# Optimization experiments

Hardware: AMD Instinct MI355X
Metric: run time of the kernel (lower is better)

The kernel has to match this reference:

```python
import jax, jax.numpy as jnp
import numpy as np

H, W = 512, 512
NUM_CLASSES = 21
THETA_ALPHA, THETA_BETA, THETA_GAMMA = 80.0, 13.0, 3.0
BILATERAL_COMPAT, SPATIAL_COMPAT = 10.0, 3.0
COMPATIBILITY = -1.0
NUM_ITERATIONS = 5


def _find_rows(rows, queries):
    """Index of each query row in `rows` (lexicographically sorted unique), -1 if absent."""
    M = rows.shape[0]
    u, inv = np.unique(np.concatenate([rows, queries], axis=0), axis=0, return_inverse=True)
    table = np.full(u.shape[0], -1, np.int64)
    table[inv[:M]] = np.arange(M)
    return table[inv[M:]].astype(np.int32)


def _perm_init(feats):
    """Permutohedral lattice init (Adams et al.).
    Returns os [N,d+1] (1-based lattice indices, 0 = pad row), ws [N,d+1] barycentric
    weights, nbrs [d+1,M,2] blur neighbor indices (1-based, 0 = missing)."""
    N, d = feats.shape
    inv_std = np.sqrt(2.0 / 3.0) * (d + 1)
    scale = inv_std / np.sqrt((np.arange(1, d + 1) * np.arange(2, d + 2)).astype(np.float64))
    cf = feats.astype(np.float64) * scale[None]
    # Elevate onto the hyperplane sum(x)=0 in d+1 dims
    E = np.zeros((N, d + 1), np.float64)
    sm = np.zeros(N, np.float64)
    for i in range(d, 0, -1):
        E[:, i] = sm - i * cf[:, i - 1]
        sm = sm + cf[:, i - 1]
    E[:, 0] = sm
    down = 1.0 / (d + 1)
    v = E * down
    up_p = np.ceil(v) * (d + 1)
    dn_p = np.floor(v) * (d + 1)
    rem0 = np.where(up_p - E < E - dn_p, up_p, dn_p)  # nearest remainder-0 point
    sum_ = np.round(rem0.sum(1) * down).astype(np.int64)
    diff = E - rem0
    order = np.argsort(-diff, axis=1, kind='stable')
    rank = np.empty((N, d + 1), np.int64)
    np.put_along_axis(rank, order, np.broadcast_to(np.arange(d + 1, dtype=np.int64), (N, d + 1)).copy(), axis=1)
    rank = rank + sum_[:, None]
    ls = rank < 0
    rank = rank + ls * (d + 1); rem0 = rem0 + ls * (d + 1)
    gt = rank > d
    rank = rank - gt * (d + 1); rem0 = rem0 - gt * (d + 1)
    # Barycentric weights
    bary = np.zeros((N, d + 2), np.float64)
    vv = (E - rem0) * down
    rows_idx = np.arange(N)[:, None]
    np.add.at(bary, (rows_idx, d - rank), vv)
    np.add.at(bary, (rows_idx, d + 1 - rank), -vv)
    bary[:, 0] += 1.0 + bary[:, d + 1]
    ws = bary[:, :d + 1].astype(np.float32)
    # Keys of the d+1 enclosing simplex vertices (first d coords only)
    rem0i = np.round(rem0[:, :d]).astype(np.int32)
    ranks = rank[:, :d]
    keys = np.empty((N, d + 1, d), np.int32)
    for k in range(d + 1):
        keys[:, k, :] = rem0i + np.where(ranks < d + 1 - k, k, k - (d + 1)).astype(np.int32)
    uniq, inv = np.unique(keys.reshape(-1, d), axis=0, return_inverse=True)
    M = uniq.shape[0]
    os_ = (inv.reshape(N, d + 1) + 1).astype(np.int32)
    # Blur neighbors along each lattice direction j
    nbrs = np.zeros((d + 1, M, 2), np.int32)
    for j in range(d + 1):
        n1 = uniq - 1; n2 = uniq + 1
        if j < d:
            n1 = n1.copy(); n2 = n2.copy()
            n1[:, j] += d + 1; n2[:, j] -= d + 1
        nbrs[j, :, 0] = _find_rows(uniq, n1) + 1
        nbrs[j, :, 1] = _find_rows(uniq, n2) + 1
    return os_, ws, nbrs


def setup_inputs() -> dict:
    key = jax.random.key(0)
    k1, k2 = jax.random.split(key)
    unary = jax.random.normal(k1, (H, W, NUM_CLASSES), jnp.float32)
    image = jax.random.uniform(k2, (H, W, 3), jnp.float32) * 255.0  # 0..255 like RGB
    ys, xs = np.meshgrid(np.arange(H, dtype=np.float32), np.arange(W, dtype=np.float32), indexing='ij')
    img = np.asarray(image)
    bifeats = np.concatenate([(xs / THETA_ALPHA)[..., None], (ys / THETA_ALPHA)[..., None], img / THETA_BETA], axis=-1).reshape(-1, 5).astype(np.float32)
    spfeats = np.concatenate([(xs / THETA_GAMMA)[..., None], (ys / THETA_GAMMA)[..., None]], axis=-1).reshape(-1, 2).astype(np.float32)
    os_bi, ws_bi, nbr_bi = _perm_init(bifeats)
    os_sp, ws_sp, nbr_sp = _perm_init(spfeats)
    return {
        'unary': unary,
        'ws_bi': jnp.asarray(ws_bi), 'ws_sp': jnp.asarray(ws_sp),
        'os_bi': jnp.asarray(os_bi), 'os_sp': jnp.asarray(os_sp),
        'nbr_bi': jnp.asarray(nbr_bi), 'nbr_sp': jnp.asarray(nbr_sp),
    }


def lattice_compute(inp, os_, ws, nbrs):
    """Permutohedral splat -> blur -> slice. inp [N,C]; os_ [N,d+1] 1-based;
    ws [N,d+1]; nbrs [d+1,M,2] 1-based with 0 = missing (maps to zero pad row)."""
    N, C = inp.shape
    d = os_.shape[1] - 1
    M = nbrs.shape[1]
    splat = (ws[..., None] * inp[:, None, :]).reshape(-1, C)  # [N*(d+1), C]
    val = jnp.zeros((M + 1, C), inp.dtype).at[os_.reshape(-1)].add(splat)

    def blur(val, nbr_j):
        mixed = val[1:] + 0.5 * (val[nbr_j[:, 0]] + val[nbr_j[:, 1]])
        return val.at[1:].set(mixed), None

    val, _ = jax.lax.scan(blur, val, nbrs)
    alpha = 1.0 / (1.0 + 2.0 ** (-d))
    return alpha * jnp.einsum('nj,njc->nc', ws, val[os_])


def reference(unary, ws_bi, ws_sp, os_bi, os_sp, nbr_bi, nbr_sp):
    N = H * W
    u = unary.reshape(N, NUM_CLASSES)
    ones = jnp.ones((N, 1), jnp.float32)
    bi_norm = 1.0 / (lattice_compute(ones, os_bi, ws_bi, nbr_bi) ** 0.5 + 1e-20)
    sp_norm = 1.0 / (lattice_compute(ones, os_sp, ws_sp, nbr_sp) ** 0.5 + 1e-20)
    Q = jax.nn.softmax(-u, axis=-1)
    for _ in range(NUM_ITERATIONS):
        bi = lattice_compute(Q * bi_norm, os_bi, ws_bi, nbr_bi) * bi_norm
        sp = lattice_compute(Q * sp_norm, os_sp, ws_sp, nbr_sp) * sp_norm
        pairwise = COMPATIBILITY * (BILATERAL_COMPAT * bi + SPATIAL_COMPAT * sp)
        Q = jax.nn.softmax(-u - pairwise, axis=-1)
    return Q.reshape(H, W, NUM_CLASSES)
```

## Files before the change

kernel.cpp:

```cpp
#include <hip/hip_runtime.h>
#include <hip/hip_fp16.h>

#define NPIX (512 * 512)
#define LOG2N 18
#define NC 21
#define CP 11
#define SCAN_CHUNK 2048
#define SCAN_T 256

static inline int cdiv_l(long a, int b) { return (int)((a + b - 1) / b); }

__global__ void histrank2_k(const int* __restrict__ osA, int* __restrict__ cntA,
                            int* __restrict__ rnkA, int NA, int KA,
                            const int* __restrict__ osB, int* __restrict__ cntB,
                            int* __restrict__ rnkB, int NB, int KB) {
    int t = blockIdx.x * blockDim.x + threadIdx.x;
    if (t < NA) {
        int j = t >> LOG2N, n = t & (NPIX - 1);
        rnkA[t] = atomicAdd(&cntA[osA[(size_t)n * KA + j]], 1);
    } else {
        int tb = t - NA;
        if (tb < NB) {
            int j = tb >> LOG2N, n = tb & (NPIX - 1);
            rnkB[tb] = atomicAdd(&cntB[osB[(size_t)n * KB + j]], 1);
        }
    }
}

__global__ void scan1d_k(const int* __restrict__ cntA, int* __restrict__ bsumA, int LA, int nbA,
                         const int* __restrict__ cntB, int* __restrict__ bsumB, int LB) {
    __shared__ int s[SCAN_T];
    int blk = blockIdx.x;
    const int* cnt; int* bsum; int L; int b;
    if (blk < nbA) { cnt = cntA; bsum = bsumA; L = LA; b = blk; }
    else           { cnt = cntB; bsum = bsumB; L = LB; b = blk - nbA; }
    int base = b * SCAN_CHUNK;
    int tsum = 0;
    for (int j = threadIdx.x; j < SCAN_CHUNK; j += SCAN_T) {
        int i = base + j;
        tsum += (i < L) ? cnt[i] : 0;
    }
    s[threadIdx.x] = tsum; __syncthreads();
    for (int o = SCAN_T / 2; o > 0; o >>= 1) {
        if (threadIdx.x < o) s[threadIdx.x] += s[threadIdx.x + o];
        __syncthreads();
    }
    if (threadIdx.x == 0) bsum[b] = s[0];
}

__global__ void scan2d_k(int* __restrict__ bsumA, int nbA, int* __restrict__ offA, int LA,
                         int* __restrict__ bsumB, int nbB, int* __restrict__ offB, int LB) {
    __shared__ int s[SCAN_T];
    int* bsum; int nb; int* off; int L;
    if (blockIdx.x == 0) { bsum = bsumA; nb = nbA; off = offA; L = LA; }
    else                 { bsum = bsumB; nb = nbB; off = offB; L = LB; }
    int tid = threadIdx.x;
    int per = (nb + SCAN_T - 1) / SCAN_T;
    int tsum = 0;
    for (int j = 0; j < per; j++) { int i = tid * per + j; if (i < nb) tsum += bsum[i]; }
    s[tid] = tsum; __syncthreads();
    for (int o = 1; o < SCAN_T; o <<= 1) {
        int v = (tid >= o) ? s[tid - o] : 0;
        __syncthreads();
        s[tid] += v;
        __syncthreads();
    }
    int excl = s[tid] - tsum;
    int total = s[SCAN_T - 1];
    int run = excl;
    for (int j = 0; j < per; j++) {
        int i = tid * per + j;
        if (i < nb) { int v = bsum[i]; bsum[i] = run; run += v; }
    }
    if (tid == 0) off[L] = total;
}

__global__ void scan3d_k(const int* __restrict__ cntA, const int* __restrict__ bsumA,
                         int* __restrict__ offA, int LA, int nbA,
                         const int* __restrict__ cntB, const int* __restrict__ bsumB,
                         int* __restrict__ offB, int LB) {
    __shared__ int s[SCAN_T];
    const int PER = SCAN_CHUNK / SCAN_T;
    int blk = blockIdx.x;
    const int* cnt; const int* bsum; int* off; int L; int b;
    if (blk < nbA) { cnt = cntA; bsum = bsumA; off = offA; L = LA; b = blk; }
    else           { cnt = cntB; bsum = bsumB; off = offB; L = LB; b = blk - nbA; }
    int tid = threadIdx.x;
    int base = b * SCAN_CHUNK + tid * PER;
    int c[PER];
    int tsum = 0;
#pragma unroll
    for (int j = 0; j < PER; j++) { int i = base + j; c[j] = (i < L) ? cnt[i] : 0; tsum += c[j]; }
    s[tid] = tsum; __syncthreads();
    for (int o = 1; o < SCAN_T; o <<= 1) {
        int v = (tid >= o) ? s[tid - o] : 0;
        __syncthreads();
        s[tid] += v;
        __syncthreads();
    }
    int run = bsum[b] + s[tid] - tsum;
#pragma unroll
    for (int j = 0; j < PER; j++) {
        int i = base + j;
        if (i < L) off[i] = run;
        run += c[j];
    }
}

__global__ void scatter2_k(const int* __restrict__ osA, const float* __restrict__ wsA,
                           const int* __restrict__ offA, const int* __restrict__ rnkA,
                           int2* __restrict__ pA, int NA, int KA,
                           const int* __restrict__ osB, const float* __restrict__ wsB,
                           const int* __restrict__ offB, const int* __restrict__ rnkB,
                           int2* __restrict__ pB, int NB, int KB) {
    int t = blockIdx.x * blockDim.x + threadIdx.x;
    if (t < NA) {
        int j = t >> LOG2N, n = t & (NPIX - 1);
        size_t e = (size_t)n * KA + j;
        int m = osA[e];
        int p = offA[m] + rnkA[t];
        pA[p] = make_int2(n, __float_as_int(wsA[e]));
    } else {
        int tb = t - NA;
        if (tb < NB) {
            int j = tb >> LOG2N, n = tb & (NPIX - 1);
            size_t e = (size_t)n * KB + j;
            int m = osB[e];
            int p = offB[m] + rnkB[tb];
            pB[p] = make_int2(n, __float_as_int(wsB[e]));
        }
    }
}

__global__ void wn2_k(int2* __restrict__ pA, const float* __restrict__ nrmA, int NA,
                      int2* __restrict__ pB, const float* __restrict__ nrmB, int NB) {
    int t = blockIdx.x * blockDim.x + threadIdx.x;
    if (t < NA) {
        int2 e = pA[t];
        e.y = __float_as_int(__int_as_float(e.y) * nrmA[e.x]);
        pA[t] = e;
    } else {
        t -= NA;
        if (t < NB) {
            int2 e = pB[t];
            e.y = __float_as_int(__int_as_float(e.y) * nrmB[e.x]);
            pB[t] = e;
        }
    }
}

__global__ void splat1d_k(const int2* __restrict__ pE_bi, const int* __restrict__ off_bi,
                          float* __restrict__ val_bi, int Mbi,
                          const int2* __restrict__ pE_sp, const int* __restrict__ off_sp,
                          float* __restrict__ val_sp, int Msp) {
    int t = blockIdx.x * blockDim.x + threadIdx.x;
    const int2* pE; const int* off; float* val; int m;
    if (t <= Mbi) { pE = pE_bi; off = off_bi; val = val_bi; m = t; }
    else {
        m = t - (Mbi + 1);
        if (m > Msp) return;
        pE = pE_sp; off = off_sp; val = val_sp;
    }
    float s = 0.f;
    if (m > 0) {
        int e0 = off[m], e1 = off[m + 1];
        for (int e = e0; e < e1; e++) s += __int_as_float(pE[e].y);
    }
    val[m] = s;
}

__global__ void blur1d_k(const float* __restrict__ biIn, float* __restrict__ biOut,
                         const int* __restrict__ nbr_bi, int Mbi,
                         const float* __restrict__ spIn, float* __restrict__ spOut,
                         const int* __restrict__ nbr_sp, int Msp) {
    int t = blockIdx.x * blockDim.x + threadIdx.x;
    if (t <= Mbi) {
        if (t == 0) { biOut[0] = 0.f; return; }
        int2 nn = ((const int2*)nbr_bi)[t - 1];
        biOut[t] = biIn[t] + 0.5f * (biIn[nn.x] + biIn[nn.y]);
    } else if (spIn) {
        int m = t - (Mbi + 1);
        if (m > Msp) return;
        if (m == 0) { spOut[0] = 0.f; return; }
        int2 nn = ((const int2*)nbr_sp)[m - 1];
        spOut[m] = spIn[m] + 0.5f * (spIn[nn.x] + spIn[nn.y]);
    }
}

__global__ void prep_k(const float* __restrict__ unary,
                       const int* __restrict__ os_bi, const float* __restrict__ ws_bi,
                       const float* __restrict__ nv_bi, float* __restrict__ nrm_bi, float abi,
                       const int* __restrict__ os_sp, const float* __restrict__ ws_sp,
                       const float* __restrict__ nv_sp, float* __restrict__ nrm_sp, float asp,
                       __half2* __restrict__ Qh, __half2* __restrict__ uh, int N) {
    int t = blockIdx.x * blockDim.x + threadIdx.x;
    if (t < N) {
        float s = 0.f;
        for (int j = 0; j < 6; j++)
            s += ws_bi[(size_t)t * 6 + j] * nv_bi[os_bi[(size_t)t * 6 + j]];
        nrm_bi[t] = 1.f / (sqrtf(abi * s) + 1e-20f);
    } else if (t < 2 * N) {
        int n = t - N;
        float s = 0.f;
        for (int j = 0; j < 3; j++)
            s += ws_sp[(size_t)n * 3 + j] * nv_sp[os_sp[(size_t)n * 3 + j]];
        nrm_sp[n] = 1.f / (sqrtf(asp * s) + 1e-20f);
    } else if (t < 3 * N) {
        int n = t - 2 * N;
        const float* up = unary + (size_t)n * NC;
        float uv[2 * CP], v[2 * CP];
        float mx = -1e30f;
#pragma unroll
        for (int c = 0; c < NC; c++) { uv[c] = up[c]; v[c] = -uv[c]; mx = fmaxf(mx, v[c]); }
        float s = 0.f;
#pragma unroll
        for (int c = 0; c < NC; c++) { v[c] = __expf(v[c] - mx); s += v[c]; }
        float inv = 1.f / s;
#pragma unroll
        for (int c = 0; c < NC; c++) v[c] *= inv;
        v[NC] = 0.f; uv[NC] = 0.f;
        __half2* hp = Qh + (size_t)n * CP;
        __half2* uhp = uh + (size_t)n * CP;
#pragma unroll
        for (int i = 0; i < CP; i++) {
            hp[i]  = __floats2half2_rn(v[2 * i], v[2 * i + 1]);
            uhp[i] = __floats2half2_rn(uv[2 * i], uv[2 * i + 1]);
        }
    }
}

__device__ __forceinline__ void splat_row(const __half2* __restrict__ Qh,
                                          const int2* __restrict__ pE, const int* __restrict__ off,
                                          __half2* __restrict__ val, int m) {
    float acc[2 * CP];
#pragma unroll
    for (int i = 0; i < 2 * CP; i++) acc[i] = 0.f;
    if (m > 0) {
        int e0 = off[m], e1 = off[m + 1];
        for (int e = e0; e < e1; e++) {
            int2 ent = pE[e];
            float w = __int_as_float(ent.y);
            const __half2* qp = Qh + (size_t)ent.x * CP;
#pragma unroll
            for (int i = 0; i < CP; i++) {
                float2 q = __half22float2(qp[i]);
                acc[2 * i]     += w * q.x;
                acc[2 * i + 1] += w * q.y;
            }
        }
    }
    __half2* vp = val + (size_t)m * CP;
#pragma unroll
    for (int i = 0; i < CP; i++)
        vp[i] = __floats2half2_rn(acc[2 * i], acc[2 * i + 1]);
}

__global__ void splatH2_k(const __half2* __restrict__ Qh,
                          const int2* __restrict__ pE_bi, const int* __restrict__ off_bi,
                          __half2* __restrict__ val_bi, int Mbi,
                          const int2* __restrict__ pE_sp, const int* __restrict__ off_sp,
                          __half2* __restrict__ val_sp, int Msp) {
    int t = blockIdx.x * blockDim.x + threadIdx.x;
    if (t <= Mbi) {
        splat_row(Qh, pE_bi, off_bi, val_bi, t);
    } else {
        int m = t - (Mbi + 1);
        if (m > Msp) return;
        splat_row(Qh, pE_sp, off_sp, val_sp, m);
    }
}

__device__ __forceinline__ void blur2_row(const __half2* __restrict__ vin, __half2* __restrict__ op,
                                          const int* __restrict__ nbrA, const int* __restrict__ nbrB,
                                          int m) {
    if (m == 0) {
        __half2 z = __floats2half2_rn(0.f, 0.f);
#pragma unroll
        for (int i = 0; i < CP; i++) op[i] = z;
        return;
    }
    float acc[2 * CP];
#pragma unroll
    for (int i = 0; i < 2 * CP; i++) acc[i] = 0.f;
    int2 nbB = ((const int2*)nbrB)[m - 1];
    {
        int2 na = ((const int2*)nbrA)[m - 1];
        const __half2* p0 = vin + (size_t)m * CP;
        const __half2* p1 = vin + (size_t)na.x * CP;
        const __half2* p2 = vin + (size_t)na.y * CP;
#pragma unroll
        for (int i = 0; i < CP; i++) {
            float2 a = __half22float2(p0[i]);
            float2 b = __half22float2(p1[i]);
            float2 c = __half22float2(p2[i]);
            acc[2 * i]     += a.x + 0.5f * (b.x + c.x);
            acc[2 * i + 1] += a.y + 0.5f * (b.y + c.y);
        }
    }
    if (nbB.x > 0) {
        int2 na = ((const int2*)nbrA)[nbB.x - 1];
        const __half2* p0 = vin + (size_t)nbB.x * CP;
        const __half2* p1 = vin + (size_t)na.x * CP;
        const __half2* p2 = vin + (size_t)na.y * CP;
#pragma unroll
        for (int i = 0; i < CP; i++) {
            float2 a = __half22float2(p0[i]);
            float2 b = __half22float2(p1[i]);
            float2 c = __half22float2(p2[i]);
            acc[2 * i]     += 0.5f * (a.x + 0.5f * (b.x + c.x));
            acc[2 * i + 1] += 0.5f * (a.y + 0.5f * (b.y + c.y));
        }
    }
    if (nbB.y > 0) {
        int2 na = ((const int2*)nbrA)[nbB.y - 1];
        const __half2* p0 = vin + (size_t)nbB.y * CP;
        const __half2* p1 = vin + (size_t)na.x * CP;
        const __half2* p2 = vin + (size_t)na.y * CP;
#pragma unroll
        for (int i = 0; i < CP; i++) {
            float2 a = __half22float2(p0[i]);
            float2 b = __half22float2(p1[i]);
            float2 c = __half22float2(p2[i]);
            acc[2 * i]     += 0.5f * (a.x + 0.5f * (b.x + c.x));
            acc[2 * i + 1] += 0.5f * (a.y + 0.5f * (b.y + c.y));
        }
    }
#pragma unroll
    for (int i = 0; i < CP; i++)
        op[i] = __floats2half2_rn(acc[2 * i], acc[2 * i + 1]);
}

__device__ __forceinline__ void blur1_row(const __half2* __restrict__ vin, __half2* __restrict__ op,
                                          const int* __restrict__ nbr, int m) {
    if (m == 0) {
        __half2 z = __floats2half2_rn(0.f, 0.f);
#pragma unroll
        for (int i = 0; i < CP; i++) op[i] = z;
        return;
    }
    int2 nn = ((const int2*)nbr)[m - 1];
    const __half2* p0 = vin + (size_t)m * CP;
    const __half2* p1 = vin + (size_t)nn.x * CP;
    const __half2* p2 = vin + (size_t)nn.y * CP;
#pragma unroll
    for (int i = 0; i < CP; i++) {
        float2 a = __half22float2(p0[i]);
        float2 b = __half22float2(p1[i]);
        float2 c = __half22float2(p2[i]);
        op[i] = __floats2half2_rn(a.x + 0.5f * (b.x + c.x), a.y + 0.5f * (b.y + c.y));
    }
}

__global__ void blurP1_k(const __half2* __restrict__ biIn, __half2* __restrict__ biOut,
                         const int* __restrict__ nA_bi, const int* __restrict__ nB_bi, int Mbi,
                         const __half2* __restrict__ spIn, __half2* __restrict__ spOut,
                         const int* __restrict__ nA_sp, const int* __restrict__ nB_sp, int Msp) {
    int t = blockIdx.x * blockDim.x + threadIdx.x;
    if (t <= Mbi) {
        blur2_row(biIn, biOut + (size_t)t * CP, nA_bi, nB_bi, t);
    } else {
        int m = t - (Mbi + 1);
        if (m > Msp) return;
        blur2_row(spIn, spOut + (size_t)m * CP, nA_sp, nB_sp, m);
    }
}

__global__ void blurP2_k(const __half2* __restrict__ biIn, __half2* __restrict__ biOut,
                         const int* __restrict__ nA_bi, const int* __restrict__ nB_bi, int Mbi,
                         const __half2* __restrict__ spIn, __half2* __restrict__ spOut,
                         const int* __restrict__ nA_sp, int Msp) {
    int t = blockIdx.x * blockDim.x + threadIdx.x;
    if (t <= Mbi) {
        blur2_row(biIn, biOut + (size_t)t * CP, nA_bi, nB_bi, t);
    } else {
        int m = t - (Mbi + 1);
        if (m > Msp) return;
        blur1_row(spIn, spOut + (size_t)m * CP, nA_sp, m);
    }
}

__global__ void blurP3_k(const __half2* __restrict__ biIn, __half2* __restrict__ biOut,
                         const int* __restrict__ nA_bi, const int* __restrict__ nB_bi, int Mbi) {
    int t = blockIdx.x * blockDim.x + threadIdx.x;
    if (t > Mbi) return;
    blur2_row(biIn, biOut + (size_t)t * CP, nA_bi, nB_bi, t);
}

__global__ void slice_update_k(const __half2* __restrict__ uh,
                               const int* __restrict__ os_bi, const float* __restrict__ ws_bi,
                               const __half2* __restrict__ vbi, const float* __restrict__ nrm_bi,
                               const int* __restrict__ os_sp, const float* __restrict__ ws_sp,
                               const __half2* __restrict__ vsp, const float* __restrict__ nrm_sp,
                               float* __restrict__ Q, __half2* __restrict__ Qh,
                               int N, float abi, float asp, int final_it) {
    int n = blockIdx.x * blockDim.x + threadIdx.x;
    if (n >= N) return;
    float acc[2 * CP];
#pragma unroll
    for (int i = 0; i < 2 * CP; i++) acc[i] = 0.f;
    for (int j = 0; j < 6; j++) {
        float w = ws_bi[(size_t)n * 6 + j];
        const __half2* vp = vbi + (size_t)os_bi[(size_t)n * 6 + j] * CP;
#pragma unroll
        for (int i = 0; i < CP; i++) {
            float2 f = __half22float2(vp[i]);
            acc[2 * i]     += w * f.x;
            acc[2 * i + 1] += w * f.y;
        }
    }
    float sb = 10.f * abi * nrm_bi[n];
#pragma unroll
    for (int i = 0; i < 2 * CP; i++) acc[i] *= sb;
    float ss = 3.f * asp * nrm_sp[n];
    for (int j = 0; j < 3; j++) {
        float w = ss * ws_sp[(size_t)n * 3 + j];
        const __half2* vp = vsp + (size_t)os_sp[(size_t)n * 3 + j] * CP;
#pragma unroll
        for (int i = 0; i < CP; i++) {
            float2 f = __half22float2(vp[i]);
            acc[2 * i]     += w * f.x;
            acc[2 * i + 1] += w * f.y;
        }
    }
    const __half2* uhp = uh + (size_t)n * CP;
#pragma unroll
    for (int i = 0; i < CP; i++) {
        float2 uu = __half22float2(uhp[i]);
        acc[2 * i]     -= uu.x;
        acc[2 * i + 1] -= uu.y;
    }
    float mx = -1e30f;
#pragma unroll
    for (int c = 0; c < NC; c++) mx = fmaxf(mx, acc[c]);
    float s = 0.f;
#pragma unroll
    for (int c = 0; c < NC; c++) { acc[c] = __expf(acc[c] - mx); s += acc[c]; }
    float inv = 1.f / s;
#pragma unroll
    for (int c = 0; c < NC; c++) acc[c] *= inv;
    acc[NC] = 0.f;
    if (final_it) {
        float* qp = Q + (size_t)n * NC;
#pragma unroll
        for (int c = 0; c < NC; c++) qp[c] = acc[c];
    } else {
        __half2* hp = Qh + (size_t)n * CP;
#pragma unroll
        for (int i = 0; i < CP; i++) hp[i] = __floats2half2_rn(acc[2 * i], acc[2 * i + 1]);
    }
}

extern "C" void kernel_launch(void* const* d_in, const int* in_sizes, int n_in,
                              void* d_out, int out_size, void* d_ws, size_t ws_size,
                              hipStream_t stream) {
    const float* unary  = (const float*)d_in[0];
    const float* ws_bi  = (const float*)d_in[1];
    const float* ws_sp  = (const float*)d_in[2];
    const int*   os_bi  = (const int*)d_in[3];
    const int*   os_sp  = (const int*)d_in[4];
    const int*   nbr_bi = (const int*)d_in[5];
    const int*   nbr_sp = (const int*)d_in[6];
    float* Q = (float*)d_out;

    const int N = NPIX, Kbi = 6, Ksp = 3;
    const int Mbi = in_sizes[5] / (Kbi * 2);
    const int Msp = in_sizes[6] / (Ksp * 2);
    const int NKbi = N * Kbi, NKsp = N * Ksp;
    const float alpha_bi = 32.f / 33.f;
    const float alpha_sp = 0.8f;

    char* basec = (char*)d_ws;
    size_t off4 = 0;
    auto allocf = [&](size_t nf) { float* p = (float*)basec + off4; off4 += (nf + 3) & ~(size_t)3; return p; };
    auto alloci = [&](size_t ni) { int* p = (int*)basec + off4; off4 += (ni + 3) & ~(size_t)3; return p; };
    auto alloch2 = [&](size_t nh2) { __half2* p = (__half2*)((float*)basec + off4); off4 += (nh2 + 3) & ~(size_t)3; return p; };
    auto alloci2 = [&](size_t ni2) { int2* p = (int2*)((float*)basec + off4); off4 += 2 * ni2; return p; };

    float*   nrm_bi = allocf(N);
    float*   nrm_sp = allocf(N);
    __half2* Qh     = alloch2((size_t)N * CP);
    __half2* uh     = alloch2((size_t)N * CP);
    int2*    pE_bi  = alloci2(NKbi);
    int*     off_bi = alloci(Mbi + 2);
    int2*    pE_sp  = alloci2(NKsp);
    int*     off_sp = alloci(Msp + 2);
    int*     cnt_bi = alloci((size_t)(Mbi + 1) + (Msp + 1));
    int*     cnt_sp = cnt_bi + (Mbi + 1);
    int*     rnk_bi = alloci(NKbi);
    int*     rnk_sp = alloci(NKsp);
    int*     bsumA  = alloci(4096);
    int*     bsumB  = alloci(4096);
    __half2* vbiA   = alloch2((size_t)(Mbi + 1) * CP);
    __half2* vbiB   = alloch2((size_t)(Mbi + 1) * CP);
    __half2* vspA   = alloch2((size_t)(Msp + 1) * CP);
    __half2* vspB   = alloch2((size_t)(Msp + 1) * CP);
    float* nv_biA = (float*)vbiA;
    float* nv_biB = (float*)vbiB;
    float* nv_spA = (float*)vspA;
    float* nv_spB = (float*)vspB;

    const int B = 256;
    const int nb_bi = cdiv_l(Mbi + 1, SCAN_CHUNK);
    const int nb_sp = cdiv_l(Msp + 1, SCAN_CHUNK);
    const size_t cnt_span = ((size_t)(Mbi + 1) + (Msp + 1)) * sizeof(int);
    const int rows2 = (Mbi + 1) + (Msp + 1);

    hipMemsetAsync(cnt_bi, 0, cnt_span, stream);
    histrank2_k<<<cdiv_l((long)NKbi + NKsp, B), B, 0, stream>>>(
        os_bi, cnt_bi, rnk_bi, NKbi, Kbi, os_sp, cnt_sp, rnk_sp, NKsp, Ksp);
    scan1d_k<<<nb_bi + nb_sp, SCAN_T, 0, stream>>>(cnt_bi, bsumA, Mbi + 1, nb_bi,
                                                   cnt_sp, bsumB, Msp + 1);
    scan2d_k<<<2, SCAN_T, 0, stream>>>(bsumA, nb_bi, off_bi, Mbi + 1,
                                       bsumB, nb_sp, off_sp, Msp + 1);
    scan3d_k<<<nb_bi + nb_sp, SCAN_T, 0, stream>>>(cnt_bi, bsumA, off_bi, Mbi + 1, nb_bi,
                                                   cnt_sp, bsumB, off_sp, Msp + 1);
    scatter2_k<<<cdiv_l((long)NKbi + NKsp, B), B, 0, stream>>>(
        os_bi, ws_bi, off_bi, rnk_bi, pE_bi, NKbi, Kbi,
        os_sp, ws_sp, off_sp, rnk_sp, pE_sp, NKsp, Ksp);

    splat1d_k<<<cdiv_l(rows2, B), B, 0, stream>>>(pE_bi, off_bi, nv_biA, Mbi,
                                                  pE_sp, off_sp, nv_spA, Msp);
    {
        float* sb = nv_biA; float* db = nv_biB;
        float* sp = nv_spA; float* dp = nv_spB;
        for (int j = 0; j < 3; j++) {
            blur1d_k<<<cdiv_l(rows2, B), B, 0, stream>>>(
                sb, db, nbr_bi + (size_t)j * Mbi * 2, Mbi,
                sp, dp, nbr_sp + (size_t)j * Msp * 2, Msp);
            float* t = sb; sb = db; db = t;
            t = sp; sp = dp; dp = t;
        }
        for (int j = 3; j < 6; j++) {
            blur1d_k<<<cdiv_l(Mbi + 1, B), B, 0, stream>>>(
                sb, db, nbr_bi + (size_t)j * Mbi * 2, Mbi,
                nullptr, nullptr, nullptr, 0);
            float* t = sb; sb = db; db = t;
        }
        prep_k<<<cdiv_l(3L * N, B), B, 0, stream>>>(
            unary, os_bi, ws_bi, sb, nrm_bi, alpha_bi,
            os_sp, ws_sp, sp, nrm_sp, alpha_sp, Qh, uh, N);
    }

    wn2_k<<<cdiv_l((long)NKbi + NKsp, B), B, 0, stream>>>(pE_bi, nrm_bi, NKbi, pE_sp, nrm_sp, NKsp);

    for (int it = 0; it < 5; it++) {
        splatH2_k<<<cdiv_l(rows2, B), B, 0, stream>>>(
            Qh, pE_bi, off_bi, vbiA, Mbi,
            pE_sp, off_sp, vspA, Msp);
        blurP1_k<<<cdiv_l(rows2, B), B, 0, stream>>>(
            vbiA, vbiB, nbr_bi + (size_t)0 * Mbi * 2, nbr_bi + (size_t)1 * Mbi * 2, Mbi,
            vspA, vspB, nbr_sp + (size_t)0 * Msp * 2, nbr_sp + (size_t)1 * Msp * 2, Msp);
        blurP2_k<<<cdiv_l(rows2, B), B, 0, stream>>>(
            vbiB, vbiA, nbr_bi + (size_t)2 * Mbi * 2, nbr_bi + (size_t)3 * Mbi * 2, Mbi,
            vspB, vspA, nbr_sp + (size_t)2 * Msp * 2, Msp);
        blurP3_k<<<cdiv_l(Mbi + 1, B), B, 0, stream>>>(
            vbiA, vbiB, nbr_bi + (size_t)4 * Mbi * 2, nbr_bi + (size_t)5 * Mbi * 2, Mbi);
        slice_update_k<<<cdiv_l(N, B), B, 0, stream>>>(
            uh, os_bi, ws_bi, vbiB, nrm_bi, os_sp, ws_sp, vspA, nrm_sp,
            Q, Qh, N, alpha_bi, alpha_sp, it == 4 ? 1 : 0);
    }
}
```

Baseline: 1.083 ms.

## Parallelize splat and blur kernels over lattice rows and channel pairs

The splat and blur kernels now launch one thread per (lattice row, half2 channel pair) instead of one thread per row, giving about eleven times more threads. Neighbor gathers become coalesced across adjacent threads reading consecutive half2 values of the same row, and per-thread register pressure drops. In exchange, each thread reloads the row's offsets, neighbor indices and splat entries, so index traffic is duplicated across the eleven channel threads, and an integer divide by CP is added per thread.

```diff
diff --git a/kernel.cpp b/kernel.cpp
--- a/kernel.cpp
+++ b/kernel.cpp
@@ -229,30 +229,21 @@
     }
 }
 
-__device__ __forceinline__ void splat_row(const __half2* __restrict__ Qh,
-                                          const int2* __restrict__ pE, const int* __restrict__ off,
-                                          __half2* __restrict__ val, int m) {
-    float acc[2 * CP];
-#pragma unroll
-    for (int i = 0; i < 2 * CP; i++) acc[i] = 0.f;
+
+__device__ __forceinline__ void splat_elem(const __half2* __restrict__ Qh,
+                                           const int2* __restrict__ pE, const int* __restrict__ off,
+                                           __half2* __restrict__ val, int m, int cp) {
+    float ax = 0.f, ay = 0.f;
     if (m > 0) {
         int e0 = off[m], e1 = off[m + 1];
         for (int e = e0; e < e1; e++) {
             int2 ent = pE[e];
             float w = __int_as_float(ent.y);
-            const __half2* qp = Qh + (size_t)ent.x * CP;
-#pragma unroll
-            for (int i = 0; i < CP; i++) {
-                float2 q = __half22float2(qp[i]);
-                acc[2 * i]     += w * q.x;
-                acc[2 * i + 1] += w * q.y;
-            }
-        }
-    }
-    __half2* vp = val + (size_t)m * CP;
-#pragma unroll
-    for (int i = 0; i < CP; i++)
-        vp[i] = __floats2half2_rn(acc[2 * i], acc[2 * i + 1]);
+            float2 q = __half22float2(Qh[(size_t)ent.x * CP + cp]);
+            ax += w * q.x; ay += w * q.y;
+        }
+    }
+    val[(size_t)m * CP + cp] = __floats2half2_rn(ax, ay);
 }
 
 __global__ void splatH2_k(const __half2* __restrict__ Qh,
@@ -261,94 +252,63 @@
                           const int2* __restrict__ pE_sp, const int* __restrict__ off_sp,
                           __half2* __restrict__ val_sp, int Msp) {
     int t = blockIdx.x * blockDim.x + threadIdx.x;
-    if (t <= Mbi) {
-        splat_row(Qh, pE_bi, off_bi, val_bi, t);
-    } else {
-        int m = t - (Mbi + 1);
-        if (m > Msp) return;
-        splat_row(Qh, pE_sp, off_sp, val_sp, m);
-    }
-}
-
-__device__ __forceinline__ void blur2_row(const __half2* __restrict__ vin, __half2* __restrict__ op,
-                                          const int* __restrict__ nbrA, const int* __restrict__ nbrB,
-                                          int m) {
-    if (m == 0) {
-        __half2 z = __floats2half2_rn(0.f, 0.f);
-#pragma unroll
-        for (int i = 0; i < CP; i++) op[i] = z;
-        return;
-    }
-    float acc[2 * CP];
-#pragma unroll
-    for (int i = 0; i < 2 * CP; i++) acc[i] = 0.f;
+    int totBi = (Mbi + 1) * CP;
+    if (t < totBi) {
+        int m = t / CP, cp = t - m * CP;
+        splat_elem(Qh, pE_bi, off_bi, val_bi, m, cp);
+    } else {
+        t -= totBi;
+        if (t >= (Msp + 1) * CP) return;
+        int m = t / CP, cp = t - m * CP;
+        splat_elem(Qh, pE_sp, off_sp, val_sp, m, cp);
+    }
+}
+
+__device__ __forceinline__ void blur2_elem(const __half2* __restrict__ vin,
+                                           __half2* __restrict__ vout,
+                                           const int* __restrict__ nbrA,
+                                           const int* __restrict__ nbrB, int m, int cp) {
+    size_t o = (size_t)m * CP + cp;
+    if (m == 0) { vout[o] = __floats2half2_rn(0.f, 0.f); return; }
     int2 nbB = ((const int2*)nbrB)[m - 1];
+    float ax, ay;
     {
         int2 na = ((const int2*)nbrA)[m - 1];
-        const __half2* p0 = vin + (size_t)m * CP;
-        const __half2* p1 = vin + (size_t)na.x * CP;
-        const __half2* p2 = vin + (size_t)na.y * CP;
-#pragma unroll
-        for (int i = 0; i < CP; i++) {
-            float2 a = __half22float2(p0[i]);
-            float2 b = __half22float2(p1[i]);
-            float2 c = __half22float2(p2[i]);
-            acc[2 * i]     += a.x + 0.5f * (b.x + c.x);
-            acc[2 * i + 1] += a.y + 0.5f * (b.y + c.y);
-        }
+        float2 a = __half22float2(vin[o]);
+        float2 b = __half22float2(vin[(size_t)na.x * CP + cp]);
+        float2 c = __half22float2(vin[(size_t)na.y * CP + cp]);
+        ax = a.x + 0.5f * (b.x + c.x);
+        ay = a.y + 0.5f * (b.y + c.y);
     }
     if (nbB.x > 0) {
         int2 na = ((const int2*)nbrA)[nbB.x - 1];
-        const __half2* p0 = vin + (size_t)nbB.x * CP;
-        const __half2* p1 = vin + (size_t)na.x * CP;
-        const __half2* p2 = vin + (size_t)na.y * CP;
-#pragma unroll
-        for (int i = 0; i < CP; i++) {
-            float2 a = __half22float2(p0[i]);
-            float2 b = __half22float2(p1[i]);
-            float2 c = __half22float2(p2[i]);
-            acc[2 * i]     += 0.5f * (a.x + 0.5f * (b.x + c.x));
-            acc[2 * i + 1] += 0.5f * (a.y + 0.5f * (b.y + c.y));
-        }
+        float2 a = __half22float2(vin[(size_t)nbB.x * CP + cp]);
+        float2 b = __half22float2(vin[(size_t)na.x * CP + cp]);
+        float2 c = __half22float2(vin[(size_t)na.y * CP + cp]);
+        ax += 0.5f * (a.x + 0.5f * (b.x + c.x));
+        ay += 0.5f * (a.y + 0.5f * (b.y + c.y));
     }
     if (nbB.y > 0) {
         int2 na = ((const int2*)nbrA)[nbB.y - 1];
-        const __half2* p0 = vin + (size_t)nbB.y * CP;
-        const __half2* p1 = vin + (size_t)na.x * CP;
-        const __half2* p2 = vin + (size_t)na.y * CP;
-#pragma unroll
-        for (int i = 0; i < CP; i++) {
-            float2 a = __half22float2(p0[i]);
-            float2 b = __half22float2(p1[i]);
-            float2 c = __half22float2(p2[i]);
-            acc[2 * i]     += 0.5f * (a.x + 0.5f * (b.x + c.x));
-            acc[2 * i + 1] += 0.5f * (a.y + 0.5f * (b.y + c.y));
-        }
-    }
-#pragma unroll
-    for (int i = 0; i < CP; i++)
-        op[i] = __floats2half2_rn(acc[2 * i], acc[2 * i + 1]);
-}
-
-__device__ __forceinline__ void blur1_row(const __half2* __restrict__ vin, __half2* __restrict__ op,
-                                          const int* __restrict__ nbr, int m) {
-    if (m == 0) {
-        __half2 z = __floats2half2_rn(0.f, 0.f);
-#pragma unroll
-        for (int i = 0; i < CP; i++) op[i] = z;
-        return;
-    }
+        float2 a = __half22float2(vin[(size_t)nbB.y * CP + cp]);
+        float2 b = __half22float2(vin[(size_t)na.x * CP + cp]);
+        float2 c = __half22float2(vin[(size_t)na.y * CP + cp]);
+        ax += 0.5f * (a.x + 0.5f * (b.x + c.x));
+        ay += 0.5f * (a.y + 0.5f * (b.y + c.y));
+    }
+    vout[o] = __floats2half2_rn(ax, ay);
+}
+
+__device__ __forceinline__ void blur1_elem(const __half2* __restrict__ vin,
+                                           __half2* __restrict__ vout,
+                                           const int* __restrict__ nbr, int m, int cp) {
+    size_t o = (size_t)m * CP + cp;
+    if (m == 0) { vout[o] = __floats2half2_rn(0.f, 0.f); return; }
     int2 nn = ((const int2*)nbr)[m - 1];
-    const __half2* p0 = vin + (size_t)m * CP;
-    const __half2* p1 = vin + (size_t)nn.x * CP;
-    const __half2* p2 = vin + (size_t)nn.y * CP;
-#pragma unroll
-    for (int i = 0; i < CP; i++) {
-        float2 a = __half22float2(p0[i]);
-        float2 b = __half22float2(p1[i]);
-        float2 c = __half22float2(p2[i]);
-        op[i] = __floats2half2_rn(a.x + 0.5f * (b.x + c.x), a.y + 0.5f * (b.y + c.y));
-    }
+    float2 a = __half22float2(vin[o]);
+    float2 b = __half22float2(vin[(size_t)nn.x * CP + cp]);
+    float2 c = __half22float2(vin[(size_t)nn.y * CP + cp]);
+    vout[o] = __floats2half2_rn(a.x + 0.5f * (b.x + c.x), a.y + 0.5f * (b.y + c.y));
 }
 
 __global__ void blurP1_k(const __half2* __restrict__ biIn, __half2* __restrict__ biOut,
@@ -356,12 +316,15 @@
                          const __half2* __restrict__ spIn, __half2* __restrict__ spOut,
                          const int* __restrict__ nA_sp, const int* __restrict__ nB_sp, int Msp) {
     int t = blockIdx.x * blockDim.x + threadIdx.x;
-    if (t <= Mbi) {
-        blur2_row(biIn, biOut + (size_t)t * CP, nA_bi, nB_bi, t);
-    } else {
-        int m = t - (Mbi + 1);
-        if (m > Msp) return;
-        blur2_row(spIn, spOut + (size_t)m * CP, nA_sp, nB_sp, m);
+    int totBi = (Mbi + 1) * CP;
+    if (t < totBi) {
+        int m = t / CP, cp = t - m * CP;
+        blur2_elem(biIn, biOut, nA_bi, nB_bi, m, cp);
+    } else {
+        t -= totBi;
+        if (t >= (Msp + 1) * CP) return;
+        int m = t / CP, cp = t - m * CP;
+        blur2_elem(spIn, spOut, nA_sp, nB_sp, m, cp);
     }
 }
 
@@ -370,20 +333,24 @@
                          const __half2* __restrict__ spIn, __half2* __restrict__ spOut,
                          const int* __restrict__ nA_sp, int Msp) {
     int t = blockIdx.x * blockDim.x + threadIdx.x;
-    if (t <= Mbi) {
-        blur2_row(biIn, biOut + (size_t)t * CP, nA_bi, nB_bi, t);
-    } else {
-        int m = t - (Mbi + 1);
-        if (m > Msp) return;
-        blur1_row(spIn, spOut + (size_t)m * CP, nA_sp, m);
+    int totBi = (Mbi + 1) * CP;
+    if (t < totBi) {
+        int m = t / CP, cp = t - m * CP;
+        blur2_elem(biIn, biOut, nA_bi, nB_bi, m, cp);
+    } else {
+        t -= totBi;
+        if (t >= (Msp + 1) * CP) return;
+        int m = t / CP, cp = t - m * CP;
+        blur1_elem(spIn, spOut, nA_sp, m, cp);
     }
 }
 
 __global__ void blurP3_k(const __half2* __restrict__ biIn, __half2* __restrict__ biOut,
                          const int* __restrict__ nA_bi, const int* __restrict__ nB_bi, int Mbi) {
     int t = blockIdx.x * blockDim.x + threadIdx.x;
-    if (t > Mbi) return;
-    blur2_row(biIn, biOut + (size_t)t * CP, nA_bi, nB_bi, t);
+    if (t >= (Mbi + 1) * CP) return;
+    int m = t / CP, cp = t - m * CP;
+    blur2_elem(biIn, biOut, nA_bi, nB_bi, m, cp);
 }
 
 __global__ void slice_update_k(const __half2* __restrict__ uh,
@@ -504,6 +471,8 @@
     const int nb_sp = cdiv_l(Msp + 1, SCAN_CHUNK);
     const size_t cnt_span = ((size_t)(Mbi + 1) + (Msp + 1)) * sizeof(int);
     const int rows2 = (Mbi + 1) + (Msp + 1);
+    const long elems2 = (long)rows2 * CP;
+    const long elemsBi = (long)(Mbi + 1) * CP;
 
     hipMemsetAsync(cnt_bi, 0, cnt_span, stream);
     histrank2_k<<<cdiv_l((long)NKbi + NKsp, B), B, 0, stream>>>(
@@ -544,16 +513,16 @@
     wn2_k<<<cdiv_l((long)NKbi + NKsp, B), B, 0, stream>>>(pE_bi, nrm_bi, NKbi, pE_sp, nrm_sp, NKsp);
 
     for (int it = 0; it < 5; it++) {
-        splatH2_k<<<cdiv_l(rows2, B), B, 0, stream>>>(
+        splatH2_k<<<cdiv_l(elems2, B), B, 0, stream>>>(
             Qh, pE_bi, off_bi, vbiA, Mbi,
             pE_sp, off_sp, vspA, Msp);
-        blurP1_k<<<cdiv_l(rows2, B), B, 0, stream>>>(
+        blurP1_k<<<cdiv_l(elems2, B), B, 0, stream>>>(
             vbiA, vbiB, nbr_bi + (size_t)0 * Mbi * 2, nbr_bi + (size_t)1 * Mbi * 2, Mbi,
             vspA, vspB, nbr_sp + (size_t)0 * Msp * 2, nbr_sp + (size_t)1 * Msp * 2, Msp);
-        blurP2_k<<<cdiv_l(rows2, B), B, 0, stream>>>(
+        blurP2_k<<<cdiv_l(elems2, B), B, 0, stream>>>(
             vbiB, vbiA, nbr_bi + (size_t)2 * Mbi * 2, nbr_bi + (size_t)3 * Mbi * 2, Mbi,
             vspB, vspA, nbr_sp + (size_t)2 * Msp * 2, Msp);
-        blurP3_k<<<cdiv_l(Mbi + 1, B), B, 0, stream>>>(
+        blurP3_k<<<cdiv_l(elemsBi, B), B, 0, stream>>>(
             vbiA, vbiB, nbr_bi + (size_t)4 * Mbi * 2, nbr_bi + (size_t)5 * Mbi * 2, Mbi);
         slice_update_k<<<cdiv_l(N, B), B, 0, stream>>>(
             uh, os_bi, ws_bi, vbiB, nrm_bi, os_sp, ws_sp, vspA, nrm_sp,
```

Result: slower. 1.268 ms (+17.0%).
